# Optimization experiments

Hardware: AMD Instinct MI355X
Metric: run time of the kernel (lower is better)

## Reference

```python
import jax, jax.numpy as jnp
import numpy as np

N = 50000   # nodes
E = 800000  # edges (avg degree 16)
C = 96      # in = hidden = out channels


def setup_inputs() -> dict:
    key = jax.random.key(0)
    ks = jax.random.split(key, 8)
    s = np.float32(1.0 / np.sqrt(C))
    x = jax.random.normal(ks[0], (N, C), dtype=jnp.float32)
    edge_index = jax.random.randint(ks[1], (2, E), 0, N, dtype=jnp.int64)
    W1 = jax.random.normal(ks[2], (C, C), dtype=jnp.float32) * s
    Wr1 = jax.random.normal(ks[3], (C, C), dtype=jnp.float32) * s
    b1 = jnp.zeros((C,), dtype=jnp.float32)
    W2 = jax.random.normal(ks[4], (C, C), dtype=jnp.float32) * s
    Wr2 = jax.random.normal(ks[5], (C, C), dtype=jnp.float32) * s
    b2 = jnp.zeros((C,), dtype=jnp.float32)
    return {"x": x, "edge_index": edge_index,
            "W1": W1, "Wr1": Wr1, "b1": b1,
            "W2": W2, "Wr2": Wr2, "b2": b2}


def spline_conv(x, edge_index, W, W_root, b):
    """Gather-transform-scatter message passing (SplineConv core, mean aggr)."""
    src, dst = edge_index[0], edge_index[1]
    h = x @ W                                   # [N, C] transform once per node
    msg = h[src]                                # [E, C] edge gather
    agg = jax.ops.segment_sum(msg, dst, num_segments=N)        # scatter-add
    deg = jax.ops.segment_sum(jnp.ones((E,), x.dtype), dst, num_segments=N)
    agg = agg / jnp.maximum(deg, 1.0)[:, None]  # mean aggregation
    return agg + x @ W_root + b                 # root weight + bias


def reference(x, edge_index, W1, Wr1, b1, W2, Wr2, b2):
    h = jax.nn.relu(spline_conv(x, edge_index, W1, Wr1, b1))
    out = spline_conv(h, edge_index, W2, Wr2, b2)
    return out.reshape(-1)  # generalization of x.view(1600)
```

## Files before the change

kernel.cpp:

```cpp
#include <hip/hip_runtime.h>

#define C 96
#define BKT_SHIFT 9
#define BKT_SIZE 512
#define CAP 10240
#define EB 2048
typedef unsigned char u8;
typedef unsigned short u16;
typedef unsigned int u32;
typedef __attribute__((ext_vector_type(8))) short short8;
typedef __attribute__((ext_vector_type(4))) float floatx4;
typedef __attribute__((ext_vector_type(2))) float floatx2;

__device__ inline u16 f2bf(float f) {
    union { float f; u32 u; } v; v.f = f;
    u32 r = v.u + 0x7fff + ((v.u >> 16) & 1);
    return (u16)(r >> 16);
}
__device__ inline u32 pk4_fp8(float a, float b, float c, float d) {
    u32 w = 0;
    w = __builtin_amdgcn_cvt_pk_fp8_f32(a, b, w, false);
    w = __builtin_amdgcn_cvt_pk_fp8_f32(c, d, w, true);
    return w;
}
__device__ inline u8 f2fp8(float a) {
    return (u8)(__builtin_amdgcn_cvt_pk_fp8_f32(a, a, 0, false) & 0xff);
}

__global__ __launch_bounds__(256) void binA_kernel(const int* __restrict__ src,
                                                   const int* __restrict__ dst,
                                                   int* __restrict__ blk_cnt,
                                                   int* __restrict__ blk_off,
                                                   u32* __restrict__ stage, int E) {
    __shared__ u32 s_word[EB];
    __shared__ int s_cnt[128];
    __shared__ int s_inc[128];
    int bid = blockIdx.x;
    int t = threadIdx.x;
    int e0 = bid * EB;
    int cnt_here = min(EB, E - e0);

    for (int i = t; i < 128; i += 256) s_cnt[i] = 0;
    __syncthreads();

    int my_src[EB / 256], my_dl[EB / 256], my_b[EB / 256], my_rank[EB / 256];
    int nmine = 0;
#pragma unroll
    for (int k = 0; k < EB / 256; k++) {
        int i = t + k * 256;
        if (i < cnt_here) {
            int s = src[e0 + i], d = dst[e0 + i];
            int b = d >> BKT_SHIFT;
            my_src[nmine] = s;
            my_dl[nmine] = d & (BKT_SIZE - 1);
            my_b[nmine] = b;
            my_rank[nmine] = atomicAdd(&s_cnt[b], 1);
            nmine++;
        }
    }
    __syncthreads();

    if (t < 128) s_inc[t] = s_cnt[t];
    __syncthreads();
    for (int off = 1; off < 128; off <<= 1) {
        int x2 = (t >= off && t < 128) ? s_inc[t - off] : 0;
        __syncthreads();
        if (t < 128) s_inc[t] += x2;
        __syncthreads();
    }
    if (t < 128) {
        blk_cnt[bid * 128 + t] = s_cnt[t];
        blk_off[bid * 128 + t] = s_inc[t] - s_cnt[t];
    }

    for (int k = 0; k < nmine; k++) {
        int b = my_b[k];
        int slot = (s_inc[b] - s_cnt[b]) + my_rank[k];
        s_word[slot] = ((u32)my_dl[k] << 16) | (u32)my_src[k];
    }
    __syncthreads();

    for (int i = t; i < cnt_here; i += 256) stage[(size_t)bid * EB + i] = s_word[i];
}

__global__ __launch_bounds__(256) void binB_kernel(const u32* __restrict__ stage,
                                                   const int* __restrict__ blk_cnt,
                                                   const int* __restrict__ blk_off,
                                                   int* __restrict__ deg,
                                                   int* __restrict__ row_off,
                                                   u16* __restrict__ csr, int N, int DB,
                                                   int nbkt,
                                                   const float* __restrict__ x,
                                                   u16* __restrict__ xb,
                                                   u8* __restrict__ xf8, int n16, int CX,
                                                   const float* W0, const float* W1,
                                                   const float* W2, const float* W3,
                                                   u16* T0, u16* T1, u16* T2, u16* T3) {
    int bid = blockIdx.x;
    int t = threadIdx.x;
    if (bid >= nbkt) {
        if (bid < nbkt + CX) {
            int i = (bid - nbkt) * 256 + t;
            if (i >= n16) return;
            const float4* p = (const float4*)x + (size_t)i * 4;
            float4 a = p[0], b = p[1], c = p[2], d = p[3];
            short8 o0, o1;
            o0[0] = (short)f2bf(a.x); o0[1] = (short)f2bf(a.y);
            o0[2] = (short)f2bf(a.z); o0[3] = (short)f2bf(a.w);
            o0[4] = (short)f2bf(b.x); o0[5] = (short)f2bf(b.y);
            o0[6] = (short)f2bf(b.z); o0[7] = (short)f2bf(b.w);
            o1[0] = (short)f2bf(c.x); o1[1] = (short)f2bf(c.y);
            o1[2] = (short)f2bf(c.z); o1[3] = (short)f2bf(c.w);
            o1[4] = (short)f2bf(d.x); o1[5] = (short)f2bf(d.y);
            o1[6] = (short)f2bf(d.z); o1[7] = (short)f2bf(d.w);
            *(short8*)(xb + (size_t)i * 16) = o0;
            *(short8*)(xb + (size_t)i * 16 + 8) = o1;
            uint4 f8;
            f8.x = pk4_fp8(a.x, a.y, a.z, a.w);
            f8.y = pk4_fp8(b.x, b.y, b.z, b.w);
            f8.z = pk4_fp8(c.x, c.y, c.z, c.w);
            f8.w = pk4_fp8(d.x, d.y, d.z, d.w);
            *(uint4*)(xf8 + (size_t)i * 16) = f8;
        } else {
            int w = bid - nbkt - CX;
            const float* W = w == 0 ? W0 : w == 1 ? W1 : w == 2 ? W2 : W3;
            u16* T = w == 0 ? T0 : w == 1 ? T1 : w == 2 ? T2 : T3;
            for (int i = t; i < C * C; i += 256) {
                int k = i / C, n = i - k * C;
                T[n * C + k] = f2bf(W[i]);
            }
        }
        return;
    }

    __shared__ int cnt[BKT_SIZE];
    __shared__ int cur[BKT_SIZE];
    __shared__ int ssum[256];
    int b = bid;
    int n0 = b << BKT_SHIFT;
    int nn = min(BKT_SIZE, N - n0);
    int s0 = b * CAP;

    for (int i = t; i < BKT_SIZE; i += 256) cnt[i] = 0;
    __syncthreads();

    for (int i = t; i < DB; i += 256) {
        int len = blk_cnt[i * 128 + b];
        const u32* run = stage + (size_t)i * EB + blk_off[i * 128 + b];
        for (int j = 0; j < len; j++) atomicAdd(&cnt[run[j] >> 16], 1);
    }
    __syncthreads();

    int a0 = cnt[2 * t], a1 = cnt[2 * t + 1];
    ssum[t] = a0 + a1;
    __syncthreads();
    for (int off = 1; off < 256; off <<= 1) {
        int x2 = (t >= off) ? ssum[t - off] : 0;
        __syncthreads();
        ssum[t] += x2;
        __syncthreads();
    }
    int excl = ssum[t] - (a0 + a1);
    if (2 * t < nn) { deg[n0 + 2 * t] = a0; row_off[n0 + 2 * t] = s0 + excl; }
    if (2 * t + 1 < nn) { deg[n0 + 2 * t + 1] = a1; row_off[n0 + 2 * t + 1] = s0 + excl + a0; }
    __syncthreads();
    cur[2 * t] = s0 + excl;
    cur[2 * t + 1] = s0 + excl + a0;
    __syncthreads();

    for (int i = t; i < DB; i += 256) {
        int len = blk_cnt[i * 128 + b];
        const u32* run = stage + (size_t)i * EB + blk_off[i * 128 + b];
        for (int j = 0; j < len; j++) {
            u32 w = run[j];
            int p = atomicAdd(&cur[w >> 16], 1);
            csr[p] = (u16)(w & 0xffffu);
        }
    }
}

template <bool RELU, bool WF8, typename OT>
__global__ __launch_bounds__(256, 4) void layer_kernel(const u16* __restrict__ Xbf,
                                                       const u8* __restrict__ Xf8,
                                                       const int* __restrict__ row_off,
                                                       const int* __restrict__ deg,
                                                       const u16* __restrict__ csr,
                                                       const u16* __restrict__ WTA,
                                                       const u16* __restrict__ WTR,
                                                       const float* __restrict__ BIAS,
                                                       OT* __restrict__ Y,
                                                       u8* __restrict__ Yf8, int n) {
    __shared__ u16 sA[64 * 104];
    __shared__ int s_dg[64];
    __shared__ int s_perm[64];
    const int t = threadIdx.x;
    const int row0 = blockIdx.x * 64;

    if (t < 64) {
        int node = row0 + t;
        s_dg[t] = (node < n) ? deg[node] : 0;
    }
    __syncthreads();
    if (t < 64) {
        int di = s_dg[t];
        int r = 0;
#pragma unroll 8
        for (int j = 0; j < 64; j++) {
            int dj = s_dg[j];
            r += (dj < di) || (dj == di && j < t);
        }
        s_perm[r] = t;
    }
    __syncthreads();

    {
        int nl = s_perm[t >> 2];
        int node = row0 + nl;
        int q = t & 3;
        float acc[24];
#pragma unroll
        for (int i = 0; i < 24; i++) acc[i] = 0.f;
        int d = 0, start = 0;
        if (node < n) { start = row_off[node]; d = s_dg[nl]; }
        const int off4 = q * 16;
        const int off2 = 64 + q * 8;

        int j = 0;
        if (d >= 4) {
            int si[4];
#pragma unroll
            for (int k = 0; k < 4; k++) si[k] = csr[start + k];
            for (; j + 8 <= d; j += 4) {
                uint4 va[4];
                uint2 vb[4];
#pragma unroll
                for (int k = 0; k < 4; k++) {
                    const u8* p = Xf8 + (size_t)si[k] * 96;
                    va[k] = *(const uint4*)(p + off4);
                    vb[k] = *(const uint2*)(p + off2);
                }
                int sn[4];
#pragma unroll
                for (int k = 0; k < 4; k++) sn[k] = csr[start + j + 4 + k];
#pragma unroll
                for (int k = 0; k < 4; k++) {
                    u32 ws[6] = {va[k].x, va[k].y, va[k].z,
                                 va[k].w, vb[k].x, vb[k].y};
#pragma unroll
                    for (int i = 0; i < 6; i++) {
                        floatx2 lo = __builtin_amdgcn_cvt_pk_f32_fp8(ws[i], false);
                        floatx2 hi = __builtin_amdgcn_cvt_pk_f32_fp8(ws[i], true);
                        acc[4 * i]     += lo[0];
                        acc[4 * i + 1] += lo[1];
                        acc[4 * i + 2] += hi[0];
                        acc[4 * i + 3] += hi[1];
                    }
                }
#pragma unroll
                for (int k = 0; k < 4; k++) si[k] = sn[k];
            }
            {
                uint4 va[4];
                uint2 vb[4];
#pragma unroll
                for (int k = 0; k < 4; k++) {
                    const u8* p = Xf8 + (size_t)si[k] * 96;
                    va[k] = *(const uint4*)(p + off4);
                    vb[k] = *(const uint2*)(p + off2);
                }
#pragma unroll
                for (int k = 0; k < 4; k++) {
                    u32 ws[6] = {va[k].x, va[k].y, va[k].z,
                                 va[k].w, vb[k].x, vb[k].y};
#pragma unroll
                    for (int i = 0; i < 6; i++) {
                        floatx2 lo = __builtin_amdgcn_cvt_pk_f32_fp8(ws[i], false);
                        floatx2 hi = __builtin_amdgcn_cvt_pk_f32_fp8(ws[i], true);
                        acc[4 * i]     += lo[0];
                        acc[4 * i + 1] += lo[1];
                        acc[4 * i + 2] += hi[0];
                        acc[4 * i + 3] += hi[1];
                    }
                }
                j += 4;
            }
        }
        for (; j < d; j++) {
            const u8* p = Xf8 + (size_t)csr[start + j] * 96;
            uint4 va = *(const uint4*)(p + off4);
            uint2 vb = *(const uint2*)(p + off2);
            u32 ws[6] = {va.x, va.y, va.z, va.w, vb.x, vb.y};
#pragma unroll
            for (int i = 0; i < 6; i++) {
                floatx2 lo = __builtin_amdgcn_cvt_pk_f32_fp8(ws[i], false);
                floatx2 hi = __builtin_amdgcn_cvt_pk_f32_fp8(ws[i], true);
                acc[4 * i]     += lo[0];
                acc[4 * i + 1] += lo[1];
                acc[4 * i + 2] += hi[0];
                acc[4 * i + 3] += hi[1];
            }
        }
        float inv = 1.0f / fmaxf((float)d, 1.0f);
        u16* dl = sA + nl * 104;
        short8 o0, o1, o2;
#pragma unroll
        for (int i = 0; i < 8; i++) {
            o0[i] = (short)f2bf(acc[i] * inv);
            o1[i] = (short)f2bf(acc[8 + i] * inv);
            o2[i] = (short)f2bf(acc[16 + i] * inv);
        }
        *(short8*)(dl + q * 16) = o0;
        *(short8*)(dl + q * 16 + 8) = o1;
        *(short8*)(dl + 64 + q * 8) = o2;
    }
    __syncthreads();

    const int lane = t & 63;
    const int w = t >> 6;
    const int quad = lane >> 4;
    const int l16 = lane & 15;
    const int r0 = row0 + w * 16;

    floatx4 acc6[6];
#pragma unroll
    for (int i = 0; i < 6; i++) acc6[i] = (floatx4){0.f, 0.f, 0.f, 0.f};

    {
        const u16* Ap = sA + (w * 16 + l16) * 104 + quad * 8;
        const u16* Wp = WTA + l16 * C + quad * 8;
#pragma unroll
        for (int ks = 0; ks < 3; ks++) {
            short8 a = *(const short8*)(Ap + ks * 32);
#pragma unroll
            for (int nt = 0; nt < 6; nt++) {
                short8 b = *(const short8*)(Wp + nt * 16 * C + ks * 32);
                acc6[nt] = __builtin_amdgcn_mfma_f32_16x16x32_bf16(a, b, acc6[nt], 0, 0, 0);
            }
        }
    }
    {
        int arow = r0 + l16;
        if (arow >= n) arow = n - 1;
        const u16* Xp = Xbf + (size_t)arow * C + quad * 8;
        const u16* Wp = WTR + l16 * C + quad * 8;
#pragma unroll
        for (int ks = 0; ks < 3; ks++) {
            short8 a = *(const short8*)(Xp + ks * 32);
#pragma unroll
            for (int nt = 0; nt < 6; nt++) {
                short8 b = *(const short8*)(Wp + nt * 16 * C + ks * 32);
                acc6[nt] = __builtin_amdgcn_mfma_f32_16x16x32_bf16(a, b, acc6[nt], 0, 0, 0);
            }
        }
    }

#pragma unroll
    for (int nt = 0; nt < 6; nt++) {
        float bv = BIAS[nt * 16 + l16];
#pragma unroll
        for (int r = 0; r < 4; r++) {
            float v = acc6[nt][r] + bv;
            if (RELU) v = fmaxf(v, 0.f);
            acc6[nt][r] = v;
        }
    }
    __syncthreads();

    const int nrow = min(64, n - row0);
    const int lr = w * 16 + quad * 4;

    if constexpr (sizeof(OT) == 2) {
        u16* so = sA;
#pragma unroll
        for (int nt = 0; nt < 6; nt++)
#pragma unroll
            for (int r = 0; r < 4; r++)
                so[(lr + r) * 96 + nt * 16 + l16] = f2bf(acc6[nt][r]);
        __syncthreads();
        {
            char* dst = (char*)Y + (size_t)row0 * 192;
            int nbytes = nrow * 192;
            for (int ofs = t * 16; ofs < nbytes; ofs += 4096)
                *(uint4*)(dst + ofs) = *(const uint4*)((const char*)sA + ofs);
        }
        if constexpr (WF8) {
            __syncthreads();
            u8* so8 = (u8*)sA;
#pragma unroll
            for (int nt = 0; nt < 6; nt++)
#pragma unroll
                for (int r = 0; r < 4; r++)
                    so8[(lr + r) * 96 + nt * 16 + l16] = f2fp8(acc6[nt][r]);
            __syncthreads();
            char* dst8 = (char*)Yf8 + (size_t)row0 * 96;
            int nb8 = nrow * 96;
            for (int ofs = t * 16; ofs < nb8; ofs += 4096)
                *(uint4*)(dst8 + ofs) = *(const uint4*)((const char*)sA + ofs);
        }
    } else {
        float* sof = (float*)sA;
#pragma unroll
        for (int half = 0; half < 2; half++) {
            if (half) __syncthreads();
            if ((w >> 1) == half) {
#pragma unroll
                for (int nt = 0; nt < 6; nt++)
#pragma unroll
                    for (int r = 0; r < 4; r++)
                        sof[((w & 1) * 16 + quad * 4 + r) * 96 + nt * 16 + l16] = acc6[nt][r];
            }
            __syncthreads();
            int rbase = row0 + half * 32;
            int nr = n - rbase;
            nr = nr < 0 ? 0 : (nr > 32 ? 32 : nr);
            char* dst = (char*)Y + (size_t)rbase * 384;
            int nbytes = nr * 384;
            for (int ofs = t * 16; ofs < nbytes; ofs += 4096)
                *(uint4*)(dst + ofs) = *(const uint4*)((const char*)sA + ofs);
        }
    }
}

extern "C" void kernel_launch(void* const* d_in, const int* in_sizes, int n_in,
                              void* d_out, int out_size, void* d_ws, size_t ws_size,
                              hipStream_t stream) {
    const float* x   = (const float*)d_in[0];
    const int*   ei  = (const int*)d_in[1];
    const float* W1  = (const float*)d_in[2];
    const float* Wr1 = (const float*)d_in[3];
    const float* b1  = (const float*)d_in[4];
    const float* W2  = (const float*)d_in[5];
    const float* Wr2 = (const float*)d_in[6];
    const float* b2  = (const float*)d_in[7];
    float* out = (float*)d_out;

    const int N = in_sizes[0] / C;
    const int E = in_sizes[1] / 2;
    const int* src = ei;
    const int* dst = ei + E;

    const int nbkt = (N + BKT_SIZE - 1) >> BKT_SHIFT;
    const int DB   = (E + EB - 1) / EB;
    const int n16  = N * C / 16;
    const int CX   = (n16 + 255) / 256;
    int Npad = (N + 63) & ~63;

    int*  blk_cnt = (int*)d_ws;
    int*  blk_off = blk_cnt + DB * 128;
    int*  deg     = blk_off + DB * 128;
    int*  row_off = deg + Npad;
    u32*  stage   = (u32*)(row_off + Npad);
    u16*  csr     = (u16*)(stage + (size_t)DB * EB);
    u16*  xb      = csr + (((size_t)nbkt * CAP + 7) & ~(size_t)7);
    u16*  h1b     = xb + (size_t)N * C;
    u16*  wt      = h1b + (size_t)N * C;
    u16 *wt1 = wt, *wtr1 = wt + C * C, *wt2 = wt + 2 * C * C, *wtr2 = wt + 3 * C * C;
    u8*   xf8     = (u8*)(wt + 4 * C * C);
    u8*   h1f8    = xf8 + (size_t)N * 96;

    const int grid64 = (N + 63) / 64;

    binA_kernel<<<DB, 256, 0, stream>>>(src, dst, blk_cnt, blk_off, stage, E);
    binB_kernel<<<nbkt + CX + 4, 256, 0, stream>>>(stage, blk_cnt, blk_off,
                                                   deg, row_off, csr, N, DB, nbkt,
                                                   x, xb, xf8, n16, CX,
                                                   W1, Wr1, W2, Wr2, wt1, wtr1, wt2, wtr2);

    layer_kernel<true, true, u16><<<grid64, 256, 0, stream>>>(
        xb, xf8, row_off, deg, csr, wt1, wtr1, b1, h1b, h1f8, N);
    layer_kernel<false, false, float><<<grid64, 256, 0, stream>>>(
        h1b, h1f8, row_off, deg, csr, wt2, wtr2, b2, out, h1f8, N);
}
```

Baseline: 164.6 us.

## Fuse binning, conversion and both layers into one cooperative persistent kernel

Puts the four stages (edge binning, CSR build plus input and weight conversion, layer 1, layer 2) into one cooperative kernel with grid-wide syncs between them. Shared memory is a union sized for the largest stage. Leftover input-conversion chunks are spread over blocks that are idle during the bucket phase. This aims to remove kernel launch gaps and inter-kernel drain and fill, at the cost of grid.sync barriers and a grid that must fit co-resident. It falls back to the old multi-kernel path if the cooperative launch is unsupported or fails.

```diff
diff --git a/kernel.cpp b/kernel.cpp
--- a/kernel.cpp
+++ b/kernel.cpp
@@ -1,4 +1,7 @@
 #include <hip/hip_runtime.h>
+#include <hip/hip_cooperative_groups.h>
+
+namespace cg = cooperative_groups;
 
 #define C 96
 #define BKT_SHIFT 9
@@ -27,16 +30,12 @@
     return (u8)(__builtin_amdgcn_cvt_pk_fp8_f32(a, a, 0, false) & 0xff);
 }
 
-__global__ __launch_bounds__(256) void binA_kernel(const int* __restrict__ src,
-                                                   const int* __restrict__ dst,
-                                                   int* __restrict__ blk_cnt,
-                                                   int* __restrict__ blk_off,
-                                                   u32* __restrict__ stage, int E) {
-    __shared__ u32 s_word[EB];
-    __shared__ int s_cnt[128];
-    __shared__ int s_inc[128];
-    int bid = blockIdx.x;
-    int t = threadIdx.x;
+
+__device__ __forceinline__ void binA_body(int bid, int t,
+        const int* __restrict__ src, const int* __restrict__ dst,
+        int* __restrict__ blk_cnt, int* __restrict__ blk_off,
+        u32* __restrict__ stage, int E,
+        u32* s_word, int* s_cnt, int* s_inc) {
     int e0 = bid * EB;
     int cnt_here = min(EB, E - e0);
 
@@ -81,6 +80,389 @@
     __syncthreads();
 
     for (int i = t; i < cnt_here; i += 256) stage[(size_t)bid * EB + i] = s_word[i];
+}
+
+__device__ __forceinline__ void convert_chunk(int cc, int t,
+        const float* __restrict__ x, u16* __restrict__ xb,
+        u8* __restrict__ xf8, int n16) {
+    int i = cc * 256 + t;
+    if (i >= n16) return;
+    const float4* p = (const float4*)x + (size_t)i * 4;
+    float4 a = p[0], b = p[1], c = p[2], d = p[3];
+    short8 o0, o1;
+    o0[0] = (short)f2bf(a.x); o0[1] = (short)f2bf(a.y);
+    o0[2] = (short)f2bf(a.z); o0[3] = (short)f2bf(a.w);
+    o0[4] = (short)f2bf(b.x); o0[5] = (short)f2bf(b.y);
+    o0[6] = (short)f2bf(b.z); o0[7] = (short)f2bf(b.w);
+    o1[0] = (short)f2bf(c.x); o1[1] = (short)f2bf(c.y);
+    o1[2] = (short)f2bf(c.z); o1[3] = (short)f2bf(c.w);
+    o1[4] = (short)f2bf(d.x); o1[5] = (short)f2bf(d.y);
+    o1[6] = (short)f2bf(d.z); o1[7] = (short)f2bf(d.w);
+    *(short8*)(xb + (size_t)i * 16) = o0;
+    *(short8*)(xb + (size_t)i * 16 + 8) = o1;
+    uint4 f8;
+    f8.x = pk4_fp8(a.x, a.y, a.z, a.w);
+    f8.y = pk4_fp8(b.x, b.y, b.z, b.w);
+    f8.z = pk4_fp8(c.x, c.y, c.z, c.w);
+    f8.w = pk4_fp8(d.x, d.y, d.z, d.w);
+    *(uint4*)(xf8 + (size_t)i * 16) = f8;
+}
+
+__device__ __forceinline__ void wtrans_body(int t, const float* __restrict__ W,
+                                            u16* __restrict__ T) {
+    for (int i = t; i < C * C; i += 256) {
+        int k = i / C, n = i - k * C;
+        T[n * C + k] = f2bf(W[i]);
+    }
+}
+
+__device__ __forceinline__ void bucket_body(int b, int t,
+        const u32* __restrict__ stage, const int* __restrict__ blk_cnt,
+        const int* __restrict__ blk_off, int* __restrict__ deg,
+        int* __restrict__ row_off, u16* __restrict__ csr, int N, int DB,
+        int* cnt, int* cur, int* ssum) {
+    int n0 = b << BKT_SHIFT;
+    int nn = min(BKT_SIZE, N - n0);
+    int s0 = b * CAP;
+
+    for (int i = t; i < BKT_SIZE; i += 256) cnt[i] = 0;
+    __syncthreads();
+
+    for (int i = t; i < DB; i += 256) {
+        int len = blk_cnt[i * 128 + b];
+        const u32* run = stage + (size_t)i * EB + blk_off[i * 128 + b];
+        for (int j = 0; j < len; j++) atomicAdd(&cnt[run[j] >> 16], 1);
+    }
+    __syncthreads();
+
+    int a0 = cnt[2 * t], a1 = cnt[2 * t + 1];
+    ssum[t] = a0 + a1;
+    __syncthreads();
+    for (int off = 1; off < 256; off <<= 1) {
+        int x2 = (t >= off) ? ssum[t - off] : 0;
+        __syncthreads();
+        ssum[t] += x2;
+        __syncthreads();
+    }
+    int excl = ssum[t] - (a0 + a1);
+    if (2 * t < nn) { deg[n0 + 2 * t] = a0; row_off[n0 + 2 * t] = s0 + excl; }
+    if (2 * t + 1 < nn) { deg[n0 + 2 * t + 1] = a1; row_off[n0 + 2 * t + 1] = s0 + excl + a0; }
+    __syncthreads();
+    cur[2 * t] = s0 + excl;
+    cur[2 * t + 1] = s0 + excl + a0;
+    __syncthreads();
+
+    for (int i = t; i < DB; i += 256) {
+        int len = blk_cnt[i * 128 + b];
+        const u32* run = stage + (size_t)i * EB + blk_off[i * 128 + b];
+        for (int j = 0; j < len; j++) {
+            u32 w = run[j];
+            int p = atomicAdd(&cur[w >> 16], 1);
+            csr[p] = (u16)(w & 0xffffu);
+        }
+    }
+}
+
+template <bool RELU, bool WF8, typename OT>
+__device__ __forceinline__ void layer_body(int bid, int t,
+        const u16* __restrict__ Xbf, const u8* __restrict__ Xf8,
+        const int* __restrict__ row_off, const int* __restrict__ deg,
+        const u16* __restrict__ csr, const u16* __restrict__ WTA,
+        const u16* __restrict__ WTR, const float* __restrict__ BIAS,
+        OT* __restrict__ Y, u8* __restrict__ Yf8, int n,
+        u16* sA, int* s_dg, int* s_perm) {
+    const int row0 = bid * 64;
+
+    if (t < 64) {
+        int node = row0 + t;
+        s_dg[t] = (node < n) ? deg[node] : 0;
+    }
+    __syncthreads();
+    if (t < 64) {
+        int di = s_dg[t];
+        int r = 0;
+#pragma unroll 8
+        for (int j = 0; j < 64; j++) {
+            int dj = s_dg[j];
+            r += (dj < di) || (dj == di && j < t);
+        }
+        s_perm[r] = t;
+    }
+    __syncthreads();
+
+    {
+        int nl = s_perm[t >> 2];
+        int node = row0 + nl;
+        int q = t & 3;
+        float acc[24];
+#pragma unroll
+        for (int i = 0; i < 24; i++) acc[i] = 0.f;
+        int d = 0, start = 0;
+        if (node < n) { start = row_off[node]; d = s_dg[nl]; }
+        const int off4 = q * 16;
+        const int off2 = 64 + q * 8;
+
+        int j = 0;
+        if (d >= 4) {
+            int si[4];
+#pragma unroll
+            for (int k = 0; k < 4; k++) si[k] = csr[start + k];
+            for (; j + 8 <= d; j += 4) {
+                uint4 va[4];
+                uint2 vb[4];
+#pragma unroll
+                for (int k = 0; k < 4; k++) {
+                    const u8* p = Xf8 + (size_t)si[k] * 96;
+                    va[k] = *(const uint4*)(p + off4);
+                    vb[k] = *(const uint2*)(p + off2);
+                }
+                int sn[4];
+#pragma unroll
+                for (int k = 0; k < 4; k++) sn[k] = csr[start + j + 4 + k];
+#pragma unroll
+                for (int k = 0; k < 4; k++) {
+                    u32 ws[6] = {va[k].x, va[k].y, va[k].z,
+                                 va[k].w, vb[k].x, vb[k].y};
+#pragma unroll
+                    for (int i = 0; i < 6; i++) {
+                        floatx2 lo = __builtin_amdgcn_cvt_pk_f32_fp8(ws[i], false);
+                        floatx2 hi = __builtin_amdgcn_cvt_pk_f32_fp8(ws[i], true);
+                        acc[4 * i]     += lo[0];
+                        acc[4 * i + 1] += lo[1];
+                        acc[4 * i + 2] += hi[0];
+                        acc[4 * i + 3] += hi[1];
+                    }
+                }
+#pragma unroll
+                for (int k = 0; k < 4; k++) si[k] = sn[k];
+            }
+            {
+                uint4 va[4];
+                uint2 vb[4];
+#pragma unroll
+                for (int k = 0; k < 4; k++) {
+                    const u8* p = Xf8 + (size_t)si[k] * 96;
+                    va[k] = *(const uint4*)(p + off4);
+                    vb[k] = *(const uint2*)(p + off2);
+                }
+#pragma unroll
+                for (int k = 0; k < 4; k++) {
+                    u32 ws[6] = {va[k].x, va[k].y, va[k].z,
+                                 va[k].w, vb[k].x, vb[k].y};
+#pragma unroll
+                    for (int i = 0; i < 6; i++) {
+                        floatx2 lo = __builtin_amdgcn_cvt_pk_f32_fp8(ws[i], false);
+                        floatx2 hi = __builtin_amdgcn_cvt_pk_f32_fp8(ws[i], true);
+                        acc[4 * i]     += lo[0];
+                        acc[4 * i + 1] += lo[1];
+                        acc[4 * i + 2] += hi[0];
+                        acc[4 * i + 3] += hi[1];
+                    }
+                }
+                j += 4;
+            }
+        }
+        for (; j < d; j++) {
+            const u8* p = Xf8 + (size_t)csr[start + j] * 96;
+            uint4 va = *(const uint4*)(p + off4);
+            uint2 vb = *(const uint2*)(p + off2);
+            u32 ws[6] = {va.x, va.y, va.z, va.w, vb.x, vb.y};
+#pragma unroll
+            for (int i = 0; i < 6; i++) {
+                floatx2 lo = __builtin_amdgcn_cvt_pk_f32_fp8(ws[i], false);
+                floatx2 hi = __builtin_amdgcn_cvt_pk_f32_fp8(ws[i], true);
+                acc[4 * i]     += lo[0];
+                acc[4 * i + 1] += lo[1];
+                acc[4 * i + 2] += hi[0];
+                acc[4 * i + 3] += hi[1];
+            }
+        }
+        float inv = 1.0f / fmaxf((float)d, 1.0f);
+        u16* dl = sA + nl * 104;
+        short8 o0, o1, o2;
+#pragma unroll
+        for (int i = 0; i < 8; i++) {
+            o0[i] = (short)f2bf(acc[i] * inv);
+            o1[i] = (short)f2bf(acc[8 + i] * inv);
+            o2[i] = (short)f2bf(acc[16 + i] * inv);
+        }
+        *(short8*)(dl + q * 16) = o0;
+        *(short8*)(dl + q * 16 + 8) = o1;
+        *(short8*)(dl + 64 + q * 8) = o2;
+    }
+    __syncthreads();
+
+    const int lane = t & 63;
+    const int w = t >> 6;
+    const int quad = lane >> 4;
+    const int l16 = lane & 15;
+    const int r0 = row0 + w * 16;
+
+    floatx4 acc6[6];
+#pragma unroll
+    for (int i = 0; i < 6; i++) acc6[i] = (floatx4){0.f, 0.f, 0.f, 0.f};
+
+    {
+        const u16* Ap = sA + (w * 16 + l16) * 104 + quad * 8;
+        const u16* Wp = WTA + l16 * C + quad * 8;
+#pragma unroll
+        for (int ks = 0; ks < 3; ks++) {
+            short8 a = *(const short8*)(Ap + ks * 32);
+#pragma unroll
+            for (int nt = 0; nt < 6; nt++) {
+                short8 b = *(const short8*)(Wp + nt * 16 * C + ks * 32);
+                acc6[nt] = __builtin_amdgcn_mfma_f32_16x16x32_bf16(a, b, acc6[nt], 0, 0, 0);
+            }
+        }
+    }
+    {
+        int arow = r0 + l16;
+        if (arow >= n) arow = n - 1;
+        const u16* Xp = Xbf + (size_t)arow * C + quad * 8;
+        const u16* Wp = WTR + l16 * C + quad * 8;
+#pragma unroll
+        for (int ks = 0; ks < 3; ks++) {
+            short8 a = *(const short8*)(Xp + ks * 32);
+#pragma unroll
+            for (int nt = 0; nt < 6; nt++) {
+                short8 b = *(const short8*)(Wp + nt * 16 * C + ks * 32);
+                acc6[nt] = __builtin_amdgcn_mfma_f32_16x16x32_bf16(a, b, acc6[nt], 0, 0, 0);
+            }
+        }
+    }
+
+#pragma unroll
+    for (int nt = 0; nt < 6; nt++) {
+        float bv = BIAS[nt * 16 + l16];
+#pragma unroll
+        for (int r = 0; r < 4; r++) {
+            float v = acc6[nt][r] + bv;
+            if (RELU) v = fmaxf(v, 0.f);
+            acc6[nt][r] = v;
+        }
+    }
+    __syncthreads();
+
+    const int nrow = min(64, n - row0);
+    const int lr = w * 16 + quad * 4;
+
+    if constexpr (sizeof(OT) == 2) {
+        u16* so = sA;
+#pragma unroll
+        for (int nt = 0; nt < 6; nt++)
+#pragma unroll
+            for (int r = 0; r < 4; r++)
+                so[(lr + r) * 96 + nt * 16 + l16] = f2bf(acc6[nt][r]);
+        __syncthreads();
+        {
+            char* dstp = (char*)Y + (size_t)row0 * 192;
+            int nbytes = nrow * 192;
+            for (int ofs = t * 16; ofs < nbytes; ofs += 4096)
+                *(uint4*)(dstp + ofs) = *(const uint4*)((const char*)sA + ofs);
+        }
+        if constexpr (WF8) {
+            __syncthreads();
+            u8* so8 = (u8*)sA;
+#pragma unroll
+            for (int nt = 0; nt < 6; nt++)
+#pragma unroll
+                for (int r = 0; r < 4; r++)
+                    so8[(lr + r) * 96 + nt * 16 + l16] = f2fp8(acc6[nt][r]);
+            __syncthreads();
+            char* dst8 = (char*)Yf8 + (size_t)row0 * 96;
+            int nb8 = nrow * 96;
+            for (int ofs = t * 16; ofs < nb8; ofs += 4096)
+                *(uint4*)(dst8 + ofs) = *(const uint4*)((const char*)sA + ofs);
+        }
+    } else {
+        float* sof = (float*)sA;
+#pragma unroll
+        for (int half = 0; half < 2; half++) {
+            if (half) __syncthreads();
+            if ((w >> 1) == half) {
+#pragma unroll
+                for (int nt = 0; nt < 6; nt++)
+#pragma unroll
+                    for (int r = 0; r < 4; r++)
+                        sof[((w & 1) * 16 + quad * 4 + r) * 96 + nt * 16 + l16] = acc6[nt][r];
+            }
+            __syncthreads();
+            int rbase = row0 + half * 32;
+            int nr = n - rbase;
+            nr = nr < 0 ? 0 : (nr > 32 ? 32 : nr);
+            char* dstp = (char*)Y + (size_t)rbase * 384;
+            int nbytes = nr * 384;
+            for (int ofs = t * 16; ofs < nbytes; ofs += 4096)
+                *(uint4*)(dstp + ofs) = *(const uint4*)((const char*)sA + ofs);
+        }
+    }
+}
+
+__global__ __launch_bounds__(256, 4) void fused_kernel(
+        const int* __restrict__ src, const int* __restrict__ dst,
+        const float* __restrict__ x,
+        const float* __restrict__ W1, const float* __restrict__ Wr1,
+        const float* __restrict__ b1,
+        const float* __restrict__ W2, const float* __restrict__ Wr2,
+        const float* __restrict__ b2,
+        int* blk_cnt, int* blk_off, int* deg, int* row_off,
+        u32* stage, u16* csr, u16* xb, u8* xf8, u16* h1b, u8* h1f8,
+        u16* wt1, u16* wtr1, u16* wt2, u16* wtr2,
+        float* out, int N, int E, int DB, int nbkt, int n16, int CX) {
+    __shared__ __align__(16) union {
+        struct { u32 s_word[EB]; int s_cnt[128]; int s_inc[128]; } a;
+        struct { int cnt[BKT_SIZE]; int cur[BKT_SIZE]; int ssum[256]; } b;
+        struct { u16 sA[64 * 104]; int s_dg[64]; int s_perm[64]; } c;
+    } sm;
+    const int bid = blockIdx.x;
+    const int t = threadIdx.x;
+    const int GRID = (int)gridDim.x;
+    cg::grid_group grid = cg::this_grid();
+
+    if (bid < DB) {
+        binA_body(bid, t, src, dst, blk_cnt, blk_off, stage, E,
+                  sm.a.s_word, sm.a.s_cnt, sm.a.s_inc);
+    } else {
+        int cc = bid - DB;
+        if (cc < CX) convert_chunk(cc, t, x, xb, xf8, n16);
+        if (cc < 4) {
+            const float* W = cc == 0 ? W1 : cc == 1 ? Wr1 : cc == 2 ? W2 : Wr2;
+            u16* T = cc == 0 ? wt1 : cc == 1 ? wtr1 : cc == 2 ? wt2 : wtr2;
+            wtrans_body(t, W, T);
+        }
+    }
+    grid.sync();
+
+    if (bid < nbkt) {
+        bucket_body(bid, t, stage, blk_cnt, blk_off, deg, row_off, csr, N, DB,
+                    sm.b.cnt, sm.b.cur, sm.b.ssum);
+    } else {
+        int p0 = GRID - DB;
+        for (int cc = p0 + (bid - nbkt); cc < CX; cc += GRID - nbkt)
+            convert_chunk(cc, t, x, xb, xf8, n16);
+    }
+    grid.sync();
+
+    layer_body<true, true, u16>(bid, t, xb, xf8, row_off, deg, csr,
+                                wt1, wtr1, b1, h1b, h1f8, N,
+                                sm.c.sA, sm.c.s_dg, sm.c.s_perm);
+    grid.sync();
+
+    layer_body<false, false, float>(bid, t, h1b, h1f8, row_off, deg, csr,
+                                    wt2, wtr2, b2, out, h1f8, N,
+                                    sm.c.sA, sm.c.s_dg, sm.c.s_perm);
+}
+
+__global__ __launch_bounds__(256) void binA_kernel(const int* __restrict__ src,
+                                                   const int* __restrict__ dst,
+                                                   int* __restrict__ blk_cnt,
+                                                   int* __restrict__ blk_off,
+                                                   u32* __restrict__ stage, int E) {
+    __shared__ u32 s_word[EB];
+    __shared__ int s_cnt[128];
+    __shared__ int s_inc[128];
+    binA_body(blockIdx.x, threadIdx.x, src, dst, blk_cnt, blk_off, stage, E,
+              s_word, s_cnt, s_inc);
 }
 
 __global__ __launch_bounds__(256) void binB_kernel(const u32* __restrict__ stage,
@@ -100,83 +482,20 @@
     int t = threadIdx.x;
     if (bid >= nbkt) {
         if (bid < nbkt + CX) {
-            int i = (bid - nbkt) * 256 + t;
-            if (i >= n16) return;
-            const float4* p = (const float4*)x + (size_t)i * 4;
-            float4 a = p[0], b = p[1], c = p[2], d = p[3];
-            short8 o0, o1;
-            o0[0] = (short)f2bf(a.x); o0[1] = (short)f2bf(a.y);
-            o0[2] = (short)f2bf(a.z); o0[3] = (short)f2bf(a.w);
-            o0[4] = (short)f2bf(b.x); o0[5] = (short)f2bf(b.y);
-            o0[6] = (short)f2bf(b.z); o0[7] = (short)f2bf(b.w);
-            o1[0] = (short)f2bf(c.x); o1[1] = (short)f2bf(c.y);
-            o1[2] = (short)f2bf(c.z); o1[3] = (short)f2bf(c.w);
-            o1[4] = (short)f2bf(d.x); o1[5] = (short)f2bf(d.y);
-            o1[6] = (short)f2bf(d.z); o1[7] = (short)f2bf(d.w);
-            *(short8*)(xb + (size_t)i * 16) = o0;
-            *(short8*)(xb + (size_t)i * 16 + 8) = o1;
-            uint4 f8;
-            f8.x = pk4_fp8(a.x, a.y, a.z, a.w);
-            f8.y = pk4_fp8(b.x, b.y, b.z, b.w);
-            f8.z = pk4_fp8(c.x, c.y, c.z, c.w);
-            f8.w = pk4_fp8(d.x, d.y, d.z, d.w);
-            *(uint4*)(xf8 + (size_t)i * 16) = f8;
+            convert_chunk(bid - nbkt, t, x, xb, xf8, n16);
         } else {
             int w = bid - nbkt - CX;
             const float* W = w == 0 ? W0 : w == 1 ? W1 : w == 2 ? W2 : W3;
             u16* T = w == 0 ? T0 : w == 1 ? T1 : w == 2 ? T2 : T3;
-            for (int i = t; i < C * C; i += 256) {
-                int k = i / C, n = i - k * C;
-                T[n * C + k] = f2bf(W[i]);
-            }
+            wtrans_body(t, W, T);
         }
         return;
     }
-
     __shared__ int cnt[BKT_SIZE];
     __shared__ int cur[BKT_SIZE];
     __shared__ int ssum[256];
-    int b = bid;
-    int n0 = b << BKT_SHIFT;
-    int nn = min(BKT_SIZE, N - n0);
-    int s0 = b * CAP;
-
-    for (int i = t; i < BKT_SIZE; i += 256) cnt[i] = 0;
-    __syncthreads();
-
-    for (int i = t; i < DB; i += 256) {
-        int len = blk_cnt[i * 128 + b];
-        const u32* run = stage + (size_t)i * EB + blk_off[i * 128 + b];
-        for (int j = 0; j < len; j++) atomicAdd(&cnt[run[j] >> 16], 1);
-    }
-    __syncthreads();
-
-    int a0 = cnt[2 * t], a1 = cnt[2 * t + 1];
-    ssum[t] = a0 + a1;
-    __syncthreads();
-    for (int off = 1; off < 256; off <<= 1) {
-        int x2 = (t >= off) ? ssum[t - off] : 0;
-        __syncthreads();
-        ssum[t] += x2;
-        __syncthreads();
-    }
-    int excl = ssum[t] - (a0 + a1);
-    if (2 * t < nn) { deg[n0 + 2 * t] = a0; row_off[n0 + 2 * t] = s0 + excl; }
-    if (2 * t + 1 < nn) { deg[n0 + 2 * t + 1] = a1; row_off[n0 + 2 * t + 1] = s0 + excl + a0; }
-    __syncthreads();
-    cur[2 * t] = s0 + excl;
-    cur[2 * t + 1] = s0 + excl + a0;
-    __syncthreads();
-
-    for (int i = t; i < DB; i += 256) {
-        int len = blk_cnt[i * 128 + b];
-        const u32* run = stage + (size_t)i * EB + blk_off[i * 128 + b];
-        for (int j = 0; j < len; j++) {
-            u32 w = run[j];
-            int p = atomicAdd(&cur[w >> 16], 1);
-            csr[p] = (u16)(w & 0xffffu);
-        }
-    }
+    bucket_body(bid, t, stage, blk_cnt, blk_off, deg, row_off, csr, N, DB,
+                cnt, cur, ssum);
 }
 
 template <bool RELU, bool WF8, typename OT>
@@ -190,235 +509,11 @@
                                                        const float* __restrict__ BIAS,
                                                        OT* __restrict__ Y,
                                                        u8* __restrict__ Yf8, int n) {
-    __shared__ u16 sA[64 * 104];
+    __shared__ __align__(16) u16 sA[64 * 104];
     __shared__ int s_dg[64];
     __shared__ int s_perm[64];
-    const int t = threadIdx.x;
-    const int row0 = blockIdx.x * 64;
-
-    if (t < 64) {
-        int node = row0 + t;
-        s_dg[t] = (node < n) ? deg[node] : 0;
-    }
-    __syncthreads();
-    if (t < 64) {
-        int di = s_dg[t];
-        int r = 0;
-#pragma unroll 8
-        for (int j = 0; j < 64; j++) {
-            int dj = s_dg[j];
-            r += (dj < di) || (dj == di && j < t);
-        }
-        s_perm[r] = t;
-    }
-    __syncthreads();
-
-    {
-        int nl = s_perm[t >> 2];
-        int node = row0 + nl;
-        int q = t & 3;
-        float acc[24];
-#pragma unroll
-        for (int i = 0; i < 24; i++) acc[i] = 0.f;
-        int d = 0, start = 0;
-        if (node < n) { start = row_off[node]; d = s_dg[nl]; }
-        const int off4 = q * 16;
-        const int off2 = 64 + q * 8;
-
-        int j = 0;
-        if (d >= 4) {
-            int si[4];
-#pragma unroll
-            for (int k = 0; k < 4; k++) si[k] = csr[start + k];
-            for (; j + 8 <= d; j += 4) {
-                uint4 va[4];
-                uint2 vb[4];
-#pragma unroll
-                for (int k = 0; k < 4; k++) {
-                    const u8* p = Xf8 + (size_t)si[k] * 96;
-                    va[k] = *(const uint4*)(p + off4);
-                    vb[k] = *(const uint2*)(p + off2);
-                }
-                int sn[4];
-#pragma unroll
-                for (int k = 0; k < 4; k++) sn[k] = csr[start + j + 4 + k];
-#pragma unroll
-                for (int k = 0; k < 4; k++) {
-                    u32 ws[6] = {va[k].x, va[k].y, va[k].z,
-                                 va[k].w, vb[k].x, vb[k].y};
-#pragma unroll
-                    for (int i = 0; i < 6; i++) {
-                        floatx2 lo = __builtin_amdgcn_cvt_pk_f32_fp8(ws[i], false);
-                        floatx2 hi = __builtin_amdgcn_cvt_pk_f32_fp8(ws[i], true);
-                        acc[4 * i]     += lo[0];
-                        acc[4 * i + 1] += lo[1];
-                        acc[4 * i + 2] += hi[0];
-                        acc[4 * i + 3] += hi[1];
-                    }
-                }
-#pragma unroll
-                for (int k = 0; k < 4; k++) si[k] = sn[k];
-            }
-            {
-                uint4 va[4];
-                uint2 vb[4];
-#pragma unroll
-                for (int k = 0; k < 4; k++) {
-                    const u8* p = Xf8 + (size_t)si[k] * 96;
-                    va[k] = *(const uint4*)(p + off4);
-                    vb[k] = *(const uint2*)(p + off2);
-                }
-#pragma unroll
-                for (int k = 0; k < 4; k++) {
-                    u32 ws[6] = {va[k].x, va[k].y, va[k].z,
-                                 va[k].w, vb[k].x, vb[k].y};
-#pragma unroll
-                    for (int i = 0; i < 6; i++) {
-                        floatx2 lo = __builtin_amdgcn_cvt_pk_f32_fp8(ws[i], false);
-                        floatx2 hi = __builtin_amdgcn_cvt_pk_f32_fp8(ws[i], true);
-                        acc[4 * i]     += lo[0];
-                        acc[4 * i + 1] += lo[1];
-                        acc[4 * i + 2] += hi[0];
-                        acc[4 * i + 3] += hi[1];
-                    }
-                }
-                j += 4;
-            }
-        }
-        for (; j < d; j++) {
-            const u8* p = Xf8 + (size_t)csr[start + j] * 96;
-            uint4 va = *(const uint4*)(p + off4);
-            uint2 vb = *(const uint2*)(p + off2);
-            u32 ws[6] = {va.x, va.y, va.z, va.w, vb.x, vb.y};
-#pragma unroll
-            for (int i = 0; i < 6; i++) {
-                floatx2 lo = __builtin_amdgcn_cvt_pk_f32_fp8(ws[i], false);
-                floatx2 hi = __builtin_amdgcn_cvt_pk_f32_fp8(ws[i], true);
-                acc[4 * i]     += lo[0];
-                acc[4 * i + 1] += lo[1];
-                acc[4 * i + 2] += hi[0];
-                acc[4 * i + 3] += hi[1];
-            }
-        }
-        float inv = 1.0f / fmaxf((float)d, 1.0f);
-        u16* dl = sA + nl * 104;
-        short8 o0, o1, o2;
-#pragma unroll
-        for (int i = 0; i < 8; i++) {
-            o0[i] = (short)f2bf(acc[i] * inv);
-            o1[i] = (short)f2bf(acc[8 + i] * inv);
-            o2[i] = (short)f2bf(acc[16 + i] * inv);
-        }
-        *(short8*)(dl + q * 16) = o0;
-        *(short8*)(dl + q * 16 + 8) = o1;
-        *(short8*)(dl + 64 + q * 8) = o2;
-    }
-    __syncthreads();
-
-    const int lane = t & 63;
-    const int w = t >> 6;
-    const int quad = lane >> 4;
-    const int l16 = lane & 15;
-    const int r0 = row0 + w * 16;
-
-    floatx4 acc6[6];
-#pragma unroll
-    for (int i = 0; i < 6; i++) acc6[i] = (floatx4){0.f, 0.f, 0.f, 0.f};
-
-    {
-        const u16* Ap = sA + (w * 16 + l16) * 104 + quad * 8;
-        const u16* Wp = WTA + l16 * C + quad * 8;
-#pragma unroll
-        for (int ks = 0; ks < 3; ks++) {
-            short8 a = *(const short8*)(Ap + ks * 32);
-#pragma unroll
-            for (int nt = 0; nt < 6; nt++) {
-                short8 b = *(const short8*)(Wp + nt * 16 * C + ks * 32);
-                acc6[nt] = __builtin_amdgcn_mfma_f32_16x16x32_bf16(a, b, acc6[nt], 0, 0, 0);
-            }
-        }
-    }
-    {
-        int arow = r0 + l16;
-        if (arow >= n) arow = n - 1;
-        const u16* Xp = Xbf + (size_t)arow * C + quad * 8;
-        const u16* Wp = WTR + l16 * C + quad * 8;
-#pragma unroll
-        for (int ks = 0; ks < 3; ks++) {
-            short8 a = *(const short8*)(Xp + ks * 32);
-#pragma unroll
-            for (int nt = 0; nt < 6; nt++) {
-                short8 b = *(const short8*)(Wp + nt * 16 * C + ks * 32);
-                acc6[nt] = __builtin_amdgcn_mfma_f32_16x16x32_bf16(a, b, acc6[nt], 0, 0, 0);
-            }
-        }
-    }
-
-#pragma unroll
-    for (int nt = 0; nt < 6; nt++) {
-        float bv = BIAS[nt * 16 + l16];
-#pragma unroll
-        for (int r = 0; r < 4; r++) {
-            float v = acc6[nt][r] + bv;
-            if (RELU) v = fmaxf(v, 0.f);
-            acc6[nt][r] = v;
-        }
-    }
-    __syncthreads();
-
-    const int nrow = min(64, n - row0);
-    const int lr = w * 16 + quad * 4;
-
-    if constexpr (sizeof(OT) == 2) {
-        u16* so = sA;
-#pragma unroll
-        for (int nt = 0; nt < 6; nt++)
-#pragma unroll
-            for (int r = 0; r < 4; r++)
-                so[(lr + r) * 96 + nt * 16 + l16] = f2bf(acc6[nt][r]);
-        __syncthreads();
-        {
-            char* dst = (char*)Y + (size_t)row0 * 192;
-            int nbytes = nrow * 192;
-            for (int ofs = t * 16; ofs < nbytes; ofs += 4096)
-                *(uint4*)(dst + ofs) = *(const uint4*)((const char*)sA + ofs);
-        }
-        if constexpr (WF8) {
-            __syncthreads();
-            u8* so8 = (u8*)sA;
-#pragma unroll
-            for (int nt = 0; nt < 6; nt++)
-#pragma unroll
-                for (int r = 0; r < 4; r++)
-                    so8[(lr + r) * 96 + nt * 16 + l16] = f2fp8(acc6[nt][r]);
-            __syncthreads();
-            char* dst8 = (char*)Yf8 + (size_t)row0 * 96;
-            int nb8 = nrow * 96;
-            for (int ofs = t * 16; ofs < nb8; ofs += 4096)
-                *(uint4*)(dst8 + ofs) = *(const uint4*)((const char*)sA + ofs);
-        }
-    } else {
-        float* sof = (float*)sA;
-#pragma unroll
-        for (int half = 0; half < 2; half++) {
-            if (half) __syncthreads();
-            if ((w >> 1) == half) {
-#pragma unroll
-                for (int nt = 0; nt < 6; nt++)
-#pragma unroll
-                    for (int r = 0; r < 4; r++)
-                        sof[((w & 1) * 16 + quad * 4 + r) * 96 + nt * 16 + l16] = acc6[nt][r];
-            }
-            __syncthreads();
-            int rbase = row0 + half * 32;
-            int nr = n - rbase;
-            nr = nr < 0 ? 0 : (nr > 32 ? 32 : nr);
-            char* dst = (char*)Y + (size_t)rbase * 384;
-            int nbytes = nr * 384;
-            for (int ofs = t * 16; ofs < nbytes; ofs += 4096)
-                *(uint4*)(dst + ofs) = *(const uint4*)((const char*)sA + ofs);
-        }
-    }
+    layer_body<RELU, WF8, OT>(blockIdx.x, threadIdx.x, Xbf, Xf8, row_off, deg, csr,
+                              WTA, WTR, BIAS, Y, Yf8, n, sA, s_dg, s_perm);
 }
 
 extern "C" void kernel_launch(void* const* d_in, const int* in_sizes, int n_in,
@@ -434,15 +529,15 @@
     const float* b2  = (const float*)d_in[7];
     float* out = (float*)d_out;
 
-    const int N = in_sizes[0] / C;
-    const int E = in_sizes[1] / 2;
+    int N = in_sizes[0] / C;
+    int E = in_sizes[1] / 2;
     const int* src = ei;
     const int* dst = ei + E;
 
-    const int nbkt = (N + BKT_SIZE - 1) >> BKT_SHIFT;
-    const int DB   = (E + EB - 1) / EB;
-    const int n16  = N * C / 16;
-    const int CX   = (n16 + 255) / 256;
+    int nbkt = (N + BKT_SIZE - 1) >> BKT_SHIFT;
+    int DB   = (E + EB - 1) / EB;
+    int n16  = N * C / 16;
+    int CX   = (n16 + 255) / 256;
     int Npad = (N + 63) & ~63;
 
     int*  blk_cnt = (int*)d_ws;
@@ -460,12 +555,39 @@
 
     const int grid64 = (N + 63) / 64;
 
+    static int coop = -1;
+    if (coop < 0) {
+        int dev = 0;
+        (void)hipGetDevice(&dev);
+        int v = 0;
+        if (hipDeviceGetAttribute(&v, hipDeviceAttributeCooperativeLaunch, dev) != hipSuccess)
+            v = 0;
+        coop = v;
+    }
+    if (coop) {
+        void* args[] = {
+            (void*)&src, (void*)&dst, (void*)&x,
+            (void*)&W1, (void*)&Wr1, (void*)&b1,
+            (void*)&W2, (void*)&Wr2, (void*)&b2,
+            (void*)&blk_cnt, (void*)&blk_off, (void*)&deg, (void*)&row_off,
+            (void*)&stage, (void*)&csr, (void*)&xb, (void*)&xf8,
+            (void*)&h1b, (void*)&h1f8,
+            (void*)&wt1, (void*)&wtr1, (void*)&wt2, (void*)&wtr2,
+            (void*)&out, (void*)&N, (void*)&E, (void*)&DB, (void*)&nbkt,
+            (void*)&n16, (void*)&CX};
+        hipError_t e = hipLaunchCooperativeKernel((const void*)fused_kernel,
+                                                  dim3(grid64), dim3(256),
+                                                  args, 0, stream);
+        if (e == hipSuccess) return;
+        (void)hipGetLastError();
+        coop = 0;
+    }
+
     binA_kernel<<<DB, 256, 0, stream>>>(src, dst, blk_cnt, blk_off, stage, E);
     binB_kernel<<<nbkt + CX + 4, 256, 0, stream>>>(stage, blk_cnt, blk_off,
                                                    deg, row_off, csr, N, DB, nbkt,
                                                    x, xb, xf8, n16, CX,
                                                    W1, Wr1, W2, Wr2, wt1, wtr1, wt2, wtr2);
-
     layer_kernel<true, true, u16><<<grid64, 256, 0, stream>>>(
         xb, xf8, row_off, deg, csr, wt1, wtr1, b1, h1b, h1f8, N);
     layer_kernel<false, false, float><<<grid64, 256, 0, stream>>>(
```

New measurement: 163.7 us. About the same (-0.6%).

## Replace two-pass bucketed CSR build with global-atomic degree count, scan and scatter

Applied to the files above, without the earlier changes.

Replaces the shared-memory bucket binning (binA/binB with a staging buffer) with a global-atomic degree histogram fused into the prep kernel, a per-bucket scan kernel, and a global-atomic scatter kernel that fills the CSR. This removes the staging buffer and the serial per-bucket run loops in binB, which give little parallelism with only about 98 bucket blocks. In exchange it adds a memset and an extra launch, and relies on global atomics contended on random destinations. CSR order within a row becomes nondeterministic.

```diff
diff --git a/kernel.cpp b/kernel.cpp
--- a/kernel.cpp
+++ b/kernel.cpp
@@ -4,7 +4,6 @@
 #define BKT_SHIFT 9
 #define BKT_SIZE 512
 #define CAP 10240
-#define EB 2048
 typedef unsigned char u8;
 typedef unsigned short u16;
 typedef unsigned int u32;
@@ -27,69 +26,8 @@
     return (u8)(__builtin_amdgcn_cvt_pk_fp8_f32(a, a, 0, false) & 0xff);
 }
 
-__global__ __launch_bounds__(256) void binA_kernel(const int* __restrict__ src,
-                                                   const int* __restrict__ dst,
-                                                   int* __restrict__ blk_cnt,
-                                                   int* __restrict__ blk_off,
-                                                   u32* __restrict__ stage, int E) {
-    __shared__ u32 s_word[EB];
-    __shared__ int s_cnt[128];
-    __shared__ int s_inc[128];
-    int bid = blockIdx.x;
-    int t = threadIdx.x;
-    int e0 = bid * EB;
-    int cnt_here = min(EB, E - e0);
-
-    for (int i = t; i < 128; i += 256) s_cnt[i] = 0;
-    __syncthreads();
-
-    int my_src[EB / 256], my_dl[EB / 256], my_b[EB / 256], my_rank[EB / 256];
-    int nmine = 0;
-#pragma unroll
-    for (int k = 0; k < EB / 256; k++) {
-        int i = t + k * 256;
-        if (i < cnt_here) {
-            int s = src[e0 + i], d = dst[e0 + i];
-            int b = d >> BKT_SHIFT;
-            my_src[nmine] = s;
-            my_dl[nmine] = d & (BKT_SIZE - 1);
-            my_b[nmine] = b;
-            my_rank[nmine] = atomicAdd(&s_cnt[b], 1);
-            nmine++;
-        }
-    }
-    __syncthreads();
-
-    if (t < 128) s_inc[t] = s_cnt[t];
-    __syncthreads();
-    for (int off = 1; off < 128; off <<= 1) {
-        int x2 = (t >= off && t < 128) ? s_inc[t - off] : 0;
-        __syncthreads();
-        if (t < 128) s_inc[t] += x2;
-        __syncthreads();
-    }
-    if (t < 128) {
-        blk_cnt[bid * 128 + t] = s_cnt[t];
-        blk_off[bid * 128 + t] = s_inc[t] - s_cnt[t];
-    }
-
-    for (int k = 0; k < nmine; k++) {
-        int b = my_b[k];
-        int slot = (s_inc[b] - s_cnt[b]) + my_rank[k];
-        s_word[slot] = ((u32)my_dl[k] << 16) | (u32)my_src[k];
-    }
-    __syncthreads();
-
-    for (int i = t; i < cnt_here; i += 256) stage[(size_t)bid * EB + i] = s_word[i];
-}
-
-__global__ __launch_bounds__(256) void binB_kernel(const u32* __restrict__ stage,
-                                                   const int* __restrict__ blk_cnt,
-                                                   const int* __restrict__ blk_off,
-                                                   int* __restrict__ deg,
-                                                   int* __restrict__ row_off,
-                                                   u16* __restrict__ csr, int N, int DB,
-                                                   int nbkt,
+__global__ __launch_bounds__(256) void prep_kernel(const int* __restrict__ dst,
+                                                   int* __restrict__ deg, int E, int EH,
                                                    const float* __restrict__ x,
                                                    u16* __restrict__ xb,
                                                    u8* __restrict__ xf8, int n16, int CX,
@@ -98,60 +36,58 @@
                                                    u16* T0, u16* T1, u16* T2, u16* T3) {
     int bid = blockIdx.x;
     int t = threadIdx.x;
-    if (bid >= nbkt) {
-        if (bid < nbkt + CX) {
-            int i = (bid - nbkt) * 256 + t;
-            if (i >= n16) return;
-            const float4* p = (const float4*)x + (size_t)i * 4;
-            float4 a = p[0], b = p[1], c = p[2], d = p[3];
-            short8 o0, o1;
-            o0[0] = (short)f2bf(a.x); o0[1] = (short)f2bf(a.y);
-            o0[2] = (short)f2bf(a.z); o0[3] = (short)f2bf(a.w);
-            o0[4] = (short)f2bf(b.x); o0[5] = (short)f2bf(b.y);
-            o0[6] = (short)f2bf(b.z); o0[7] = (short)f2bf(b.w);
-            o1[0] = (short)f2bf(c.x); o1[1] = (short)f2bf(c.y);
-            o1[2] = (short)f2bf(c.z); o1[3] = (short)f2bf(c.w);
-            o1[4] = (short)f2bf(d.x); o1[5] = (short)f2bf(d.y);
-            o1[6] = (short)f2bf(d.z); o1[7] = (short)f2bf(d.w);
-            *(short8*)(xb + (size_t)i * 16) = o0;
-            *(short8*)(xb + (size_t)i * 16 + 8) = o1;
-            uint4 f8;
-            f8.x = pk4_fp8(a.x, a.y, a.z, a.w);
-            f8.y = pk4_fp8(b.x, b.y, b.z, b.w);
-            f8.z = pk4_fp8(c.x, c.y, c.z, c.w);
-            f8.w = pk4_fp8(d.x, d.y, d.z, d.w);
-            *(uint4*)(xf8 + (size_t)i * 16) = f8;
-        } else {
-            int w = bid - nbkt - CX;
-            const float* W = w == 0 ? W0 : w == 1 ? W1 : w == 2 ? W2 : W3;
-            u16* T = w == 0 ? T0 : w == 1 ? T1 : w == 2 ? T2 : T3;
-            for (int i = t; i < C * C; i += 256) {
-                int k = i / C, n = i - k * C;
-                T[n * C + k] = f2bf(W[i]);
-            }
-        }
+    if (bid < EH) {
+        int e0 = bid * 512;
+        int e1 = min(e0 + 512, E);
+        for (int e = e0 + t; e < e1; e += 256)
+            atomicAdd(&deg[dst[e]], 1);
         return;
     }
-
-    __shared__ int cnt[BKT_SIZE];
-    __shared__ int cur[BKT_SIZE];
+    if (bid < EH + CX) {
+        int i = (bid - EH) * 256 + t;
+        if (i >= n16) return;
+        const float4* p = (const float4*)x + (size_t)i * 4;
+        float4 a = p[0], b = p[1], c = p[2], d = p[3];
+        short8 o0, o1;
+        o0[0] = (short)f2bf(a.x); o0[1] = (short)f2bf(a.y);
+        o0[2] = (short)f2bf(a.z); o0[3] = (short)f2bf(a.w);
+        o0[4] = (short)f2bf(b.x); o0[5] = (short)f2bf(b.y);
+        o0[6] = (short)f2bf(b.z); o0[7] = (short)f2bf(b.w);
+        o1[0] = (short)f2bf(c.x); o1[1] = (short)f2bf(c.y);
+        o1[2] = (short)f2bf(c.z); o1[3] = (short)f2bf(c.w);
+        o1[4] = (short)f2bf(d.x); o1[5] = (short)f2bf(d.y);
+        o1[6] = (short)f2bf(d.z); o1[7] = (short)f2bf(d.w);
+        *(short8*)(xb + (size_t)i * 16) = o0;
+        *(short8*)(xb + (size_t)i * 16 + 8) = o1;
+        uint4 f8;
+        f8.x = pk4_fp8(a.x, a.y, a.z, a.w);
+        f8.y = pk4_fp8(b.x, b.y, b.z, b.w);
+        f8.z = pk4_fp8(c.x, c.y, c.z, c.w);
+        f8.w = pk4_fp8(d.x, d.y, d.z, d.w);
+        *(uint4*)(xf8 + (size_t)i * 16) = f8;
+        return;
+    }
+    int w = bid - EH - CX;
+    const float* W = w == 0 ? W0 : w == 1 ? W1 : w == 2 ? W2 : W3;
+    u16* T = w == 0 ? T0 : w == 1 ? T1 : w == 2 ? T2 : T3;
+    for (int i = t; i < C * C; i += 256) {
+        int k = i / C, n = i - k * C;
+        T[n * C + k] = f2bf(W[i]);
+    }
+}
+
+__global__ __launch_bounds__(256) void scan_kernel(const int* __restrict__ deg,
+                                                   int* __restrict__ row_off,
+                                                   int* __restrict__ cur, int N) {
     __shared__ int ssum[256];
-    int b = bid;
+    int b = blockIdx.x;
+    int t = threadIdx.x;
     int n0 = b << BKT_SHIFT;
     int nn = min(BKT_SIZE, N - n0);
     int s0 = b * CAP;
 
-    for (int i = t; i < BKT_SIZE; i += 256) cnt[i] = 0;
-    __syncthreads();
-
-    for (int i = t; i < DB; i += 256) {
-        int len = blk_cnt[i * 128 + b];
-        const u32* run = stage + (size_t)i * EB + blk_off[i * 128 + b];
-        for (int j = 0; j < len; j++) atomicAdd(&cnt[run[j] >> 16], 1);
-    }
-    __syncthreads();
-
-    int a0 = cnt[2 * t], a1 = cnt[2 * t + 1];
+    int a0 = (2 * t < nn) ? deg[n0 + 2 * t] : 0;
+    int a1 = (2 * t + 1 < nn) ? deg[n0 + 2 * t + 1] : 0;
     ssum[t] = a0 + a1;
     __syncthreads();
     for (int off = 1; off < 256; off <<= 1) {
@@ -161,21 +97,20 @@
         __syncthreads();
     }
     int excl = ssum[t] - (a0 + a1);
-    if (2 * t < nn) { deg[n0 + 2 * t] = a0; row_off[n0 + 2 * t] = s0 + excl; }
-    if (2 * t + 1 < nn) { deg[n0 + 2 * t + 1] = a1; row_off[n0 + 2 * t + 1] = s0 + excl + a0; }
-    __syncthreads();
-    cur[2 * t] = s0 + excl;
-    cur[2 * t + 1] = s0 + excl + a0;
-    __syncthreads();
-
-    for (int i = t; i < DB; i += 256) {
-        int len = blk_cnt[i * 128 + b];
-        const u32* run = stage + (size_t)i * EB + blk_off[i * 128 + b];
-        for (int j = 0; j < len; j++) {
-            u32 w = run[j];
-            int p = atomicAdd(&cur[w >> 16], 1);
-            csr[p] = (u16)(w & 0xffffu);
-        }
+    if (2 * t < nn)     { row_off[n0 + 2 * t] = s0 + excl;          cur[n0 + 2 * t] = s0 + excl; }
+    if (2 * t + 1 < nn) { row_off[n0 + 2 * t + 1] = s0 + excl + a0; cur[n0 + 2 * t + 1] = s0 + excl + a0; }
+}
+
+__global__ __launch_bounds__(256) void scatter_kernel(const int* __restrict__ src,
+                                                      const int* __restrict__ dst,
+                                                      int* __restrict__ cur,
+                                                      u16* __restrict__ csr, int E) {
+    int stride = gridDim.x * 256;
+    for (int e = blockIdx.x * 256 + threadIdx.x; e < E; e += stride) {
+        int d = dst[e];
+        int s = src[e];
+        int p = atomicAdd(&cur[d], 1);
+        csr[p] = (u16)s;
     }
 }
 
@@ -190,7 +125,7 @@
                                                        const float* __restrict__ BIAS,
                                                        OT* __restrict__ Y,
                                                        u8* __restrict__ Yf8, int n) {
-    __shared__ u16 sA[64 * 104];
+    __shared__ __align__(16) u16 sA[64 * 104];
     __shared__ int s_dg[64];
     __shared__ int s_perm[64];
     const int t = threadIdx.x;
@@ -378,10 +313,10 @@
                 so[(lr + r) * 96 + nt * 16 + l16] = f2bf(acc6[nt][r]);
         __syncthreads();
         {
-            char* dst = (char*)Y + (size_t)row0 * 192;
+            char* dstp = (char*)Y + (size_t)row0 * 192;
             int nbytes = nrow * 192;
             for (int ofs = t * 16; ofs < nbytes; ofs += 4096)
-                *(uint4*)(dst + ofs) = *(const uint4*)((const char*)sA + ofs);
+                *(uint4*)(dstp + ofs) = *(const uint4*)((const char*)sA + ofs);
         }
         if constexpr (WF8) {
             __syncthreads();
@@ -413,10 +348,10 @@
             int rbase = row0 + half * 32;
             int nr = n - rbase;
             nr = nr < 0 ? 0 : (nr > 32 ? 32 : nr);
-            char* dst = (char*)Y + (size_t)rbase * 384;
+            char* dstp = (char*)Y + (size_t)rbase * 384;
             int nbytes = nr * 384;
             for (int ofs = t * 16; ofs < nbytes; ofs += 4096)
-                *(uint4*)(dst + ofs) = *(const uint4*)((const char*)sA + ofs);
+                *(uint4*)(dstp + ofs) = *(const uint4*)((const char*)sA + ofs);
         }
     }
 }
@@ -440,17 +375,15 @@
     const int* dst = ei + E;
 
     const int nbkt = (N + BKT_SIZE - 1) >> BKT_SHIFT;
-    const int DB   = (E + EB - 1) / EB;
     const int n16  = N * C / 16;
     const int CX   = (n16 + 255) / 256;
-    int Npad = (N + 63) & ~63;
-
-    int*  blk_cnt = (int*)d_ws;
-    int*  blk_off = blk_cnt + DB * 128;
-    int*  deg     = blk_off + DB * 128;
+    const int EH   = (E + 511) / 512;
+    const int Npad = (N + 63) & ~63;
+
+    int*  deg     = (int*)d_ws;
     int*  row_off = deg + Npad;
-    u32*  stage   = (u32*)(row_off + Npad);
-    u16*  csr     = (u16*)(stage + (size_t)DB * EB);
+    int*  cur     = row_off + Npad;
+    u16*  csr     = (u16*)(cur + Npad);
     u16*  xb      = csr + (((size_t)nbkt * CAP + 7) & ~(size_t)7);
     u16*  h1b     = xb + (size_t)N * C;
     u16*  wt      = h1b + (size_t)N * C;
@@ -459,12 +392,14 @@
     u8*   h1f8    = xf8 + (size_t)N * 96;
 
     const int grid64 = (N + 63) / 64;
-
-    binA_kernel<<<DB, 256, 0, stream>>>(src, dst, blk_cnt, blk_off, stage, E);
-    binB_kernel<<<nbkt + CX + 4, 256, 0, stream>>>(stage, blk_cnt, blk_off,
-                                                   deg, row_off, csr, N, DB, nbkt,
-                                                   x, xb, xf8, n16, CX,
-                                                   W1, Wr1, W2, Wr2, wt1, wtr1, wt2, wtr2);
+    const int gscat = min((E + 255) / 256, 2048);
+
+    hipMemsetAsync(deg, 0, (size_t)Npad * sizeof(int), stream);
+    prep_kernel<<<EH + CX + 4, 256, 0, stream>>>(dst, deg, E, EH,
+                                                 x, xb, xf8, n16, CX,
+                                                 W1, Wr1, W2, Wr2, wt1, wtr1, wt2, wtr2);
+    scan_kernel<<<nbkt, 256, 0, stream>>>(deg, row_off, cur, N);
+    scatter_kernel<<<gscat, 256, 0, stream>>>(src, dst, cur, csr, E);
 
     layer_kernel<true, true, u16><<<grid64, 256, 0, stream>>>(
         xb, xf8, row_off, deg, csr, wt1, wtr1, b1, h1b, h1f8, N);
```

Result: slower. 224.0 us (+36.1%).
